# Kernel tuning notes

Hardware: AMD Instinct MI355X
Metric: run time of the kernel (lower is better)

Reference implementation:

```python
import jax, jax.numpy as jnp
import numpy as np

N_NODES = 100000
N_EDGES = 1600000
F_IN = 128
HID = 128
N_GRAPHS = 1024


def setup_inputs() -> dict:
    key = jax.random.key(0)
    ks = jax.random.split(key, 20)
    x = jax.random.normal(ks[0], (N_NODES, F_IN), dtype=jnp.float32)
    edge_index = jax.random.randint(ks[1], (2, N_EDGES), 0, N_NODES, dtype=jnp.int64)
    batch = jnp.sort(jax.random.randint(ks[2], (N_NODES,), 0, N_GRAPHS, dtype=jnp.int64))
    def lin(k, fi, fo):
        s = 1.0 / np.sqrt(fi)
        return jax.random.uniform(k, (fi, fo), jnp.float32, -s, s)
    params = {
        'W1': lin(ks[3], F_IN, HID), 'b1': jnp.zeros((HID,), jnp.float32),
        'W2': lin(ks[4], HID, HID), 'b2': jnp.zeros((HID,), jnp.float32),
        'W3': lin(ks[5], HID, HID), 'b3': jnp.zeros((HID,), jnp.float32),
        'W4': lin(ks[6], HID, HID), 'b4': jnp.zeros((HID,), jnp.float32),
        'W5': lin(ks[7], HID, HID), 'b5': jnp.zeros((HID,), jnp.float32),
        'beta1': jnp.ones((1,), jnp.float32),
        'beta2': jnp.ones((1,), jnp.float32),
        'Wl': lin(ks[8], HID, 1), 'bl': jnp.zeros((1,), jnp.float32),
    }
    return {'x': x, 'edge_index': edge_index, 'batch': batch, **params}


def _forward(x, src, dst, batch, W1, b1, W2, b2, W3, b3, W4, b4, W5, b5, beta1, beta2, Wl, bl):
    N = x.shape[0]
    # symmetric GCN normalization over A + I (shared by all GCNConv layers)
    deg = jax.ops.segment_sum(jnp.ones_like(dst, dtype=x.dtype), dst, num_segments=N)
    d_is = jnp.where(deg > 0, jax.lax.rsqrt(deg), 0.0)
    norm = d_is[src] * d_is[dst]  # [E+N]

    def gcn(h, W, b):
        m = (h @ W)[src] * norm[:, None]          # per-edge messages
        return jax.ops.segment_sum(m, dst, num_segments=N) + b

    def agnn(h, beta):
        nrm = jnp.maximum(jnp.linalg.norm(h, axis=1, keepdims=True), 1e-12)
        hn = h / nrm
        alpha = beta[0] * jnp.sum(hn[src] * hn[dst], axis=1)  # cosine sim per edge
        amax = jax.ops.segment_max(alpha, dst, num_segments=N)
        e = jnp.exp(alpha - amax[dst])
        denom = jax.ops.segment_sum(e, dst, num_segments=N)
        w = e / denom[dst]
        return jax.ops.segment_sum(h[src] * w[:, None], dst, num_segments=N)

    h = jnp.tanh(gcn(x, W1, b1))
    h = jnp.tanh(gcn(h, W2, b2))
    h = jnp.tanh(gcn(h, W3, b3))
    h = jnp.tanh(gcn(h, W4, b4))
    h = jnp.tanh(gcn(h, W5, b5))
    h = jnp.tanh(agnn(h, beta1))
    h = jnp.tanh(agnn(h, beta2))

    # global mean pool per graph
    sums = jax.ops.segment_sum(h, batch, num_segments=N_GRAPHS)
    cnts = jax.ops.segment_sum(jnp.ones((N,), h.dtype), batch, num_segments=N_GRAPHS)
    pooled = sums / jnp.maximum(cnts, 1.0)[:, None]

    # layer_norm over feature dim, no affine
    mu = jnp.mean(pooled, axis=-1, keepdims=True)
    var = jnp.mean(jnp.square(pooled - mu), axis=-1, keepdims=True)
    ln = (pooled - mu) * jax.lax.rsqrt(var + 1e-5)
    # dropout is identity in eval mode
    return ln @ Wl + bl


def reference(x, edge_index, batch, W1, b1, W2, b2, W3, b3, W4, b4, W5, b5, beta1, beta2, Wl, bl):
    N = x.shape[0]
    loops = jnp.arange(N, dtype=edge_index.dtype)
    src = jnp.concatenate([edge_index[0], loops])  # add self-loops (GCNConv & AGNNConv default)
    dst = jnp.concatenate([edge_index[1], loops])
    return _forward(x, src, dst, batch, W1, b1, W2, b2, W3, b3, W4, b4, W5, b5, beta1, beta2, Wl, bl)
```

## Files before the change

kernel.cpp:

```cpp
#include <hip/hip_runtime.h>
#include <hip/hip_fp16.h>
#include <math.h>

typedef _Float16 f16x8 __attribute__((ext_vector_type(8)));
typedef float f32x4 __attribute__((ext_vector_type(4)));

union U4H8 { uint4 u; f16x8 h; };

__device__ __forceinline__ void unpack8(uint4 u, float* f) {
    union { uint4 u; __half2 h2[4]; } U; U.u = u;
    float2 a = __half22float2(U.h2[0]);
    float2 b = __half22float2(U.h2[1]);
    float2 c = __half22float2(U.h2[2]);
    float2 d = __half22float2(U.h2[3]);
    f[0] = a.x; f[1] = a.y; f[2] = b.x; f[3] = b.y;
    f[4] = c.x; f[5] = c.y; f[6] = d.x; f[7] = d.y;
}

__global__ void k_zero_deg(int* deg, int N) {
    int i = blockIdx.x * blockDim.x + threadIdx.x;
    if (i < N) deg[i] = 0;
}

__global__ void k_count(const int* __restrict__ dst, int* deg, int* rank, int E) {
    int i = blockIdx.x * blockDim.x + threadIdx.x;
    if (i < E) rank[i] = atomicAdd(&deg[dst[i]], 1);
}

__global__ void k_dis(const int* __restrict__ deg, float* dis, int N) {
    int i = blockIdx.x * blockDim.x + threadIdx.x;
    if (i < N) dis[i] = rsqrtf((float)(deg[i] + 1));
}

__global__ void k_scan1(const int* __restrict__ deg, int* part, int N) {
    int base = blockIdx.x * 1024;
    int tid = threadIdx.x;
    int s = 0;
#pragma unroll
    for (int j = 0; j < 4; ++j) {
        int idx = base + tid * 4 + j;
        if (idx < N) s += deg[idx] + 1;
    }
    __shared__ int sm[256];
    sm[tid] = s;
    __syncthreads();
    for (int off = 128; off > 0; off >>= 1) {
        if (tid < off) sm[tid] += sm[tid + off];
        __syncthreads();
    }
    if (tid == 0) part[blockIdx.x] = sm[0];
}

__global__ void k_scan2(int* part, int nb, int* offs, int N) {
    if (blockIdx.x == 0 && threadIdx.x == 0) {
        int run = 0;
        for (int b = 0; b < nb; ++b) { int t = part[b]; part[b] = run; run += t; }
        offs[N] = run;
    }
}

__global__ void k_scan3(const int* __restrict__ deg, const int* __restrict__ part,
                        int* offs, int N) {
    __shared__ int sm[256];
    int base = blockIdx.x * 1024;
    int tid = threadIdx.x;
    int a[4];
    int s = 0;
#pragma unroll
    for (int j = 0; j < 4; ++j) {
        int idx = base + tid * 4 + j;
        a[j] = (idx < N) ? (deg[idx] + 1) : 0;
        s += a[j];
    }
    sm[tid] = s;
    __syncthreads();
    for (int off = 1; off < 256; off <<= 1) {
        int v = (tid >= off) ? sm[tid - off] : 0;
        __syncthreads();
        sm[tid] += v;
        __syncthreads();
    }
    int excl = sm[tid] - s + part[blockIdx.x];
#pragma unroll
    for (int j = 0; j < 4; ++j) {
        int idx = base + tid * 4 + j;
        if (idx < N) offs[idx] = excl;
        excl += a[j];
    }
}

__global__ void k_fill_edges(const int* __restrict__ ei, int E,
                             const int* __restrict__ offs,
                             const int* __restrict__ rank, int* csr) {
    int i = blockIdx.x * blockDim.x + threadIdx.x;
    if (i >= E) return;
    int s = ei[i], d = ei[E + i];
    csr[offs[d] + rank[i]] = s;
}

__global__ void k_fill_loops(const int* __restrict__ offs, int* csr, int N) {
    int n = blockIdx.x * blockDim.x + threadIdx.x;
    if (n < N) csr[offs[n + 1] - 1] = n;
}

__global__ void k_gstart(const int* __restrict__ batch, int N, int* gstart, int G) {
    int g = blockIdx.x * blockDim.x + threadIdx.x;
    if (g > G) return;
    int lo = 0, hi = N;
    while (lo < hi) {
        int mid = (lo + hi) >> 1;
        if (batch[mid] < g) lo = mid + 1; else hi = mid;
    }
    gstart[g] = lo;
}

__global__ __launch_bounds__(256) void k_cast(
    const float* __restrict__ x, const float* __restrict__ dis,
    __half* __restrict__ hx, int npairs)
{
    int i = blockIdx.x * blockDim.x + threadIdx.x;
    if (i >= npairs) return;
    float2 v = ((const float2*)x)[i];
    float d = dis[i >> 6];
    ((__half2*)hx)[i] = __floats2half2_rn(d * v.x, d * v.y);
}

__global__ void k_prepw(const float* __restrict__ W, __half* __restrict__ wt_hi,
                        __half* __restrict__ wt_lo) {
    int t = blockIdx.x * 256 + threadIdx.x;
    int j = t & 7, q = t >> 3;
    int l15 = q & 15, nt = (q >> 4) & 7;
    int lg = (q >> 7) & 3, ks = q >> 9;
    int n = nt * 16 + l15, k = ks * 32 + lg * 8 + j;
    float w = W[k * 128 + n];
    __half hi = __float2half_rn(w);
    wt_hi[t] = hi;
    wt_lo[t] = __float2half_rn(w - __half2float(hi));
}

__global__ __launch_bounds__(256) void k_gcn_agg(
    const __half* __restrict__ g, const int* __restrict__ csr,
    const int* __restrict__ offs, const float* __restrict__ dis,
    __half* __restrict__ agg, int N)
{
    int node = (blockIdx.x * blockDim.x + threadIdx.x) >> 4;
    int l = threadIdx.x & 15;
    if (node >= N) return;
    int j0 = offs[node], j1 = offs[node + 1];
    float dd = dis[node];
    const uint4* hp = (const uint4*)g + l;
    float acc[8] = {0.f, 0.f, 0.f, 0.f, 0.f, 0.f, 0.f, 0.f};
    int j = j0;
    for (; j + 4 <= j1; j += 4) {
        int s0 = csr[j + 0], s1 = csr[j + 1], s2 = csr[j + 2], s3 = csr[j + 3];
        uint4 u0 = hp[(size_t)s0 * 16];
        uint4 u1 = hp[(size_t)s1 * 16];
        uint4 u2 = hp[(size_t)s2 * 16];
        uint4 u3 = hp[(size_t)s3 * 16];
        float f0[8], f1[8], f2[8], f3[8];
        unpack8(u0, f0); unpack8(u1, f1); unpack8(u2, f2); unpack8(u3, f3);
#pragma unroll
        for (int i = 0; i < 8; ++i)
            acc[i] += f0[i] + f1[i] + f2[i] + f3[i];
    }
    for (; j < j1; ++j) {
        int s = csr[j];
        uint4 u = hp[(size_t)s * 16];
        float f[8]; unpack8(u, f);
#pragma unroll
        for (int i = 0; i < 8; ++i) acc[i] += f[i];
    }
    union { uint4 u; __half2 h2[4]; } P;
    P.h2[0] = __floats2half2_rn(dd * acc[0], dd * acc[1]);
    P.h2[1] = __floats2half2_rn(dd * acc[2], dd * acc[3]);
    P.h2[2] = __floats2half2_rn(dd * acc[4], dd * acc[5]);
    P.h2[3] = __floats2half2_rn(dd * acc[6], dd * acc[7]);
    ((uint4*)agg)[(size_t)node * 16 + l] = P.u;
}

#define GEMM_STG_OFF 65536
#define GEMM_STG_STRIDE 72
#define GEMM_LDS_BYTES (65536 + 8 * 16 * GEMM_STG_STRIDE)

__global__ __launch_bounds__(512) void k_gemm_mfma(
    const __half* __restrict__ in, const __half* __restrict__ wt_hi,
    const __half* __restrict__ wt_lo, const float* __restrict__ bias,
    const float* __restrict__ scale, __half* __restrict__ out,
    int ntiles, int nrows, float* __restrict__ invn_out)
{
    extern __shared__ char smem[];
    uint4* wlds = (uint4*)smem;
    int tid = threadIdx.x;
    int wv = tid >> 6;
    char* stg = smem + GEMM_STG_OFF + wv * 16 * GEMM_STG_STRIDE;

    {
        const uint4* sh = (const uint4*)wt_hi;
        const uint4* sl = (const uint4*)wt_lo;
        for (int t = tid; t < 2048; t += 512) {
            wlds[t] = sh[t];
            wlds[t + 2048] = sl[t];
        }
    }
    __syncthreads();

    int lane = tid & 63;
    int l15 = lane & 15, lg = lane >> 4;

    f32x4 bv[8];
#pragma unroll
    for (int nt = 0; nt < 8; ++nt)
        bv[nt] = *(const f32x4*)(bias + nt * 16 + lg * 4);

    int wid = blockIdx.x * 8 + wv;
    int t0 = wid * 2;
    for (int tile = t0; tile < t0 + 2 && tile < ntiles; ++tile) {
        int row0 = tile * 16;
        int row = row0 + l15;
        if (row >= nrows) row = nrows - 1;

        U4H8 b[4];
        const uint4* ap = (const uint4*)(in + (size_t)row * 128);
#pragma unroll
        for (int ks = 0; ks < 4; ++ks) b[ks].u = ap[ks * 4 + lg];

        f32x4 acc[8];
#pragma unroll
        for (int nt = 0; nt < 8; ++nt) acc[nt] = (f32x4){0.f, 0.f, 0.f, 0.f};

#pragma unroll
        for (int ks = 0; ks < 4; ++ks) {
#pragma unroll
            for (int nt = 0; nt < 8; ++nt) {
                int fi = (ks * 4 + lg) * 128 + nt * 16 + l15;
                U4H8 ah; ah.u = wlds[fi];
                U4H8 al; al.u = wlds[fi + 2048];
                acc[nt] = __builtin_amdgcn_mfma_f32_16x16x32_f16(ah.h, b[ks].h, acc[nt], 0, 0, 0);
                acc[nt] = __builtin_amdgcn_mfma_f32_16x16x32_f16(al.h, b[ks].h, acc[nt], 0, 0, 0);
            }
        }

        float sc = scale ? scale[row] : 1.0f;
        float sq = 0.f;
        int node = lane >> 2, sub = lane & 3;
#pragma unroll
        for (int np = 0; np < 4; ++np) {
#pragma unroll
            for (int h = 0; h < 2; ++h) {
                int nt = np * 2 + h;
                float o[4];
#pragma unroll
                for (int r = 0; r < 4; ++r) {
                    float xv = acc[nt][r] + bv[nt][r];
                    float e = __expf(xv + xv);
                    o[r] = 1.f - 2.f / (e + 1.f);
                    sq += o[r] * o[r];
                }
                union { __half2 h2[2]; uint2 u; } pk;
                pk.h2[0] = __floats2half2_rn(sc * o[0], sc * o[1]);
                pk.h2[1] = __floats2half2_rn(sc * o[2], sc * o[3]);
                *(uint2*)(stg + l15 * GEMM_STG_STRIDE + h * 32 + lg * 8) = pk.u;
            }
            uint4 v = *(const uint4*)(stg + node * GEMM_STG_STRIDE + sub * 16);
            if (row0 + node < nrows)
                *(uint4*)(out + (size_t)(row0 + node) * 128 + np * 32 + sub * 8) = v;
        }
        if (invn_out) {
            sq += __shfl_xor(sq, 16, 64);
            sq += __shfl_xor(sq, 32, 64);
            if (lg == 0) invn_out[row] = 1.0f / fmaxf(sqrtf(sq), 1e-12f);
        }
    }
}

__global__ __launch_bounds__(256) void k_agnn(
    const __half* __restrict__ h, const int* __restrict__ csr,
    const int* __restrict__ offs, const float* __restrict__ invn,
    const float* __restrict__ beta_p, __half* __restrict__ out, int N,
    float* __restrict__ invn_out)
{
    int node = (blockIdx.x * blockDim.x + threadIdx.x) >> 4;
    int l = threadIdx.x & 15;
    if (node >= N) return;
    int j0 = offs[node], j1 = offs[node + 1];
    const uint4* hp = (const uint4*)h + l;
    float hd[8]; unpack8(hp[(size_t)node * 16], hd);
    float bi = beta_p[0] * invn[node];
    float denom = 0.f;
    float acc[8] = {0.f, 0.f, 0.f, 0.f, 0.f, 0.f, 0.f, 0.f};
    int j = j0;
    for (; j + 2 <= j1; j += 2) {
        int s0 = csr[j], s1 = csr[j + 1];
        float in0 = invn[s0], in1 = invn[s1];
        uint4 u0 = hp[(size_t)s0 * 16];
        uint4 u1 = hp[(size_t)s1 * 16];
        float f0[8], f1[8];
        unpack8(u0, f0); unpack8(u1, f1);
        float d0 = 0.f, d1 = 0.f;
#pragma unroll
        for (int i = 0; i < 8; ++i) { d0 += f0[i] * hd[i]; d1 += f1[i] * hd[i]; }
#pragma unroll
        for (int off = 1; off < 16; off <<= 1) {
            d0 += __shfl_xor(d0, off, 64);
            d1 += __shfl_xor(d1, off, 64);
        }
        float p0 = __expf(bi * in0 * d0);
        float p1 = __expf(bi * in1 * d1);
        denom += p0 + p1;
#pragma unroll
        for (int i = 0; i < 8; ++i) acc[i] += p0 * f0[i] + p1 * f1[i];
    }
    for (; j < j1; ++j) {
        int s = csr[j];
        float ins = invn[s];
        uint4 u = hp[(size_t)s * 16];
        float f[8]; unpack8(u, f);
        float d = 0.f;
#pragma unroll
        for (int i = 0; i < 8; ++i) d += f[i] * hd[i];
#pragma unroll
        for (int off = 1; off < 16; off <<= 1) d += __shfl_xor(d, off, 64);
        float p = __expf(bi * ins * d);
        denom += p;
#pragma unroll
        for (int i = 0; i < 8; ++i) acc[i] += p * f[i];
    }
    float inv = 1.0f / denom;
    float o[8];
#pragma unroll
    for (int i = 0; i < 8; ++i) o[i] = tanhf(acc[i] * inv);
    union { uint4 u; __half2 h2[4]; } P;
    P.h2[0] = __floats2half2_rn(o[0], o[1]);
    P.h2[1] = __floats2half2_rn(o[2], o[3]);
    P.h2[2] = __floats2half2_rn(o[4], o[5]);
    P.h2[3] = __floats2half2_rn(o[6], o[7]);
    ((uint4*)out)[(size_t)node * 16 + l] = P.u;
    if (invn_out) {
        float s2 = 0.f;
#pragma unroll
        for (int i = 0; i < 8; ++i) s2 += o[i] * o[i];
#pragma unroll
        for (int off = 1; off < 16; off <<= 1) s2 += __shfl_xor(s2, off, 64);
        if (l == 0) invn_out[node] = 1.0f / fmaxf(sqrtf(s2), 1e-12f);
    }
}

__global__ __launch_bounds__(256) void k_pool(
    const __half* __restrict__ h, const int* __restrict__ gstart,
    const float* __restrict__ Wl, const float* __restrict__ bl,
    float* __restrict__ out, int G)
{
    int g = (blockIdx.x * blockDim.x + threadIdx.x) >> 4;
    int l = threadIdx.x & 15;
    if (g >= G) return;
    int s = gstart[g], e = gstart[g + 1];
    const uint4* hp = (const uint4*)h + l;
    float acc[8] = {0.f, 0.f, 0.f, 0.f, 0.f, 0.f, 0.f, 0.f};
    for (int n = s; n < e; ++n) {
        float f[8]; unpack8(hp[(size_t)n * 16], f);
#pragma unroll
        for (int i = 0; i < 8; ++i) acc[i] += f[i];
    }
    float inv = 1.0f / fmaxf((float)(e - s), 1.0f);
#pragma unroll
    for (int i = 0; i < 8; ++i) acc[i] *= inv;
    float part = 0.f;
#pragma unroll
    for (int i = 0; i < 8; ++i) part += acc[i];
#pragma unroll
    for (int off = 1; off < 16; off <<= 1) part += __shfl_xor(part, off, 64);
    float mu = part * (1.0f / 128.0f);
    float vpart = 0.f;
#pragma unroll
    for (int i = 0; i < 8; ++i) { float d = acc[i] - mu; vpart += d * d; }
#pragma unroll
    for (int off = 1; off < 16; off <<= 1) vpart += __shfl_xor(vpart, off, 64);
    float r = rsqrtf(vpart * (1.0f / 128.0f) + 1e-5f);
    float4 w0 = *(const float4*)(Wl + l * 8);
    float4 w1 = *(const float4*)(Wl + l * 8 + 4);
    float wv[8] = {w0.x, w0.y, w0.z, w0.w, w1.x, w1.y, w1.z, w1.w};
    float dot = 0.f;
#pragma unroll
    for (int i = 0; i < 8; ++i) dot += (acc[i] - mu) * r * wv[i];
#pragma unroll
    for (int off = 1; off < 16; off <<= 1) dot += __shfl_xor(dot, off, 64);
    if (l == 0) out[g] = dot + bl[0];
}

extern "C" void kernel_launch(void* const* d_in, const int* in_sizes, int n_in,
                              void* d_out, int out_size, void* d_ws, size_t ws_size,
                              hipStream_t stream) {
    const float* x  = (const float*)d_in[0];
    const int* ei   = (const int*)d_in[1];
    const int* batch = (const int*)d_in[2];
    const float* Ws[5] = {(const float*)d_in[3], (const float*)d_in[5],
                          (const float*)d_in[7], (const float*)d_in[9],
                          (const float*)d_in[11]};
    const float* bs[5] = {(const float*)d_in[4], (const float*)d_in[6],
                          (const float*)d_in[8], (const float*)d_in[10],
                          (const float*)d_in[12]};
    const float* beta1 = (const float*)d_in[13];
    const float* beta2 = (const float*)d_in[14];
    const float* Wl = (const float*)d_in[15];
    const float* bl = (const float*)d_in[16];
    float* out = (float*)d_out;

    int N = in_sizes[0] / 128;
    int E = in_sizes[1] / 2;
    int G = out_size;

    char* ws = (char*)d_ws;
    size_t off = 0;
    auto alloc = [&](size_t bytes) -> void* {
        void* p = ws + off;
        off = (off + bytes + 255) & ~(size_t)255;
        return p;
    };
    __half* aggh = (__half*)alloc((size_t)N * 128 * 2);
    __half* hA   = (__half*)alloc((size_t)N * 128 * 2);
    __half* hB   = (__half*)alloc((size_t)N * 128 * 2);
    int*   deg   = (int*)alloc((size_t)N * 4);
    int*   offs  = (int*)alloc((size_t)(N + 1) * 4);
    int*   rank  = (int*)alloc((size_t)E * 4);
    int*   csr   = (int*)alloc((size_t)(E + N) * 4);
    float* dis   = (float*)alloc((size_t)N * 4);
    float* invn  = (float*)alloc((size_t)N * 4);
    float* invn2 = (float*)alloc((size_t)N * 4);
    __half* wtHi = (__half*)alloc((size_t)5 * 16384 * 2);
    __half* wtLo = (__half*)alloc((size_t)5 * 16384 * 2);
    int nb = (N + 1023) / 1024;
    int*   part  = (int*)alloc((size_t)nb * 4);
    int*   gst   = (int*)alloc((size_t)(G + 1) * 4);

    k_zero_deg<<<(N + 255) / 256, 256, 0, stream>>>(deg, N);
    k_count<<<(E + 255) / 256, 256, 0, stream>>>(ei + E, deg, rank, E);
    k_dis<<<(N + 255) / 256, 256, 0, stream>>>(deg, dis, N);
    k_scan1<<<nb, 256, 0, stream>>>(deg, part, N);
    k_scan2<<<1, 64, 0, stream>>>(part, nb, offs, N);
    k_scan3<<<nb, 256, 0, stream>>>(deg, part, offs, N);
    k_fill_edges<<<(E + 255) / 256, 256, 0, stream>>>(ei, E, offs, rank, csr);
    k_fill_loops<<<(N + 255) / 256, 256, 0, stream>>>(offs, csr, N);
    k_gstart<<<(G + 1 + 255) / 256, 256, 0, stream>>>(batch, N, gst, G);
    k_cast<<<(N * 64 + 255) / 256, 256, 0, stream>>>(x, dis, hA, N * 64);
    for (int l = 0; l < 5; ++l)
        k_prepw<<<64, 256, 0, stream>>>(Ws[l], wtHi + l * 16384, wtLo + l * 16384);

    int aggBlocks = (N + 15) / 16;
    int ntiles = (N + 15) / 16;
    int gemmBlocks = (ntiles + 15) / 16;

    const __half* hin = hA;
    __half* hout = hB;
    for (int l = 0; l < 5; ++l) {
        k_gcn_agg<<<aggBlocks, 256, 0, stream>>>(hin, csr, offs, dis, aggh, N);
        k_gemm_mfma<<<gemmBlocks, 512, GEMM_LDS_BYTES, stream>>>(
            aggh, wtHi + l * 16384, wtLo + l * 16384, bs[l],
            (l < 4) ? dis : nullptr, hout, ntiles, N,
            (l == 4) ? invn : nullptr);
        const __half* t = hin; hin = hout; hout = (__half*)t;
    }
    k_agnn<<<aggBlocks, 256, 0, stream>>>(hin, csr, offs, invn, beta1, hout, N, invn2);
    k_agnn<<<aggBlocks, 256, 0, stream>>>(hout, csr, offs, invn2, beta2, (__half*)hin, N, nullptr);
    k_pool<<<(G + 15) / 16, 256, 0, stream>>>(hin, gst, Wl, bl, out, G);
}
```

Baseline: 744.8 us.

## Assign a full wavefront per node in GCN and AGNN gather kernels

Both neighbor-aggregation kernels now map one 64-lane wavefront per node instead of 16 lanes. The four 16-lane slots each process two neighbors per iteration and then combine partial sums via cross-lane shuffles. The aim is more outstanding gathers per node and lower per-node latency in these memory-bound kernels. In exchange, lanes are masked on tail iterations and there are four times as many waves. The AGNN padding adds tiny exp(-100) terms to the softmax denominator.

```diff
diff --git a/kernel.cpp b/kernel.cpp
--- a/kernel.cpp
+++ b/kernel.cpp
@@ -6,6 +6,7 @@
 typedef float f32x4 __attribute__((ext_vector_type(4)));
 
 union U4H8 { uint4 u; f16x8 h; };
+union U4H { uint4 u; __half h[8]; __half2 h2[4]; };
 
 __device__ __forceinline__ void unpack8(uint4 u, float* f) {
     union { uint4 u; __half2 h2[4]; } U; U.u = u;
@@ -143,39 +144,42 @@
     const int* __restrict__ offs, const float* __restrict__ dis,
     __half* __restrict__ agg, int N)
 {
-    int node = (blockIdx.x * blockDim.x + threadIdx.x) >> 4;
-    int l = threadIdx.x & 15;
+    int node = (blockIdx.x * blockDim.x + threadIdx.x) >> 6;
+    int lane = threadIdx.x & 63;
+    int l15 = lane & 15, slot = lane >> 4;
     if (node >= N) return;
     int j0 = offs[node], j1 = offs[node + 1];
     float dd = dis[node];
-    const uint4* hp = (const uint4*)g + l;
+    const uint4* h4 = (const uint4*)g;
     float acc[8] = {0.f, 0.f, 0.f, 0.f, 0.f, 0.f, 0.f, 0.f};
-    int j = j0;
-    for (; j + 4 <= j1; j += 4) {
-        int s0 = csr[j + 0], s1 = csr[j + 1], s2 = csr[j + 2], s3 = csr[j + 3];
-        uint4 u0 = hp[(size_t)s0 * 16];
-        uint4 u1 = hp[(size_t)s1 * 16];
-        uint4 u2 = hp[(size_t)s2 * 16];
-        uint4 u3 = hp[(size_t)s3 * 16];
-        float f0[8], f1[8], f2[8], f3[8];
-        unpack8(u0, f0); unpack8(u1, f1); unpack8(u2, f2); unpack8(u3, f3);
-#pragma unroll
-        for (int i = 0; i < 8; ++i)
-            acc[i] += f0[i] + f1[i] + f2[i] + f3[i];
-    }
-    for (; j < j1; ++j) {
-        int s = csr[j];
-        uint4 u = hp[(size_t)s * 16];
-        float f[8]; unpack8(u, f);
-#pragma unroll
-        for (int i = 0; i < 8; ++i) acc[i] += f[i];
-    }
-    union { uint4 u; __half2 h2[4]; } P;
-    P.h2[0] = __floats2half2_rn(dd * acc[0], dd * acc[1]);
-    P.h2[1] = __floats2half2_rn(dd * acc[2], dd * acc[3]);
-    P.h2[2] = __floats2half2_rn(dd * acc[4], dd * acc[5]);
-    P.h2[3] = __floats2half2_rn(dd * acc[6], dd * acc[7]);
-    ((uint4*)agg)[(size_t)node * 16 + l] = P.u;
+    for (int jb = j0; jb < j1; jb += 8) {
+        int i0 = jb + slot * 2, i1 = i0 + 1;
+        bool v0 = i0 < j1, v1 = i1 < j1;
+        int c0 = v0 ? i0 : j0, c1 = v1 ? i1 : j0;
+        int s0 = csr[c0], s1 = csr[c1];
+        uint4 u0 = h4[(unsigned)(s0 * 16 + l15)];
+        uint4 u1 = h4[(unsigned)(s1 * 16 + l15)];
+        float m0 = v0 ? 1.f : 0.f, m1 = v1 ? 1.f : 0.f;
+        U4H A, B; A.u = u0; B.u = u1;
+#pragma unroll
+        for (int i = 0; i < 8; ++i) {
+            acc[i] = fmaf(__half2float(A.h[i]), m0, acc[i]);
+            acc[i] = fmaf(__half2float(B.h[i]), m1, acc[i]);
+        }
+    }
+#pragma unroll
+    for (int i = 0; i < 8; ++i) {
+        acc[i] += __shfl_xor(acc[i], 16, 64);
+        acc[i] += __shfl_xor(acc[i], 32, 64);
+    }
+    if (slot == 0) {
+        union { uint4 u; __half2 h2[4]; } P;
+        P.h2[0] = __floats2half2_rn(dd * acc[0], dd * acc[1]);
+        P.h2[1] = __floats2half2_rn(dd * acc[2], dd * acc[3]);
+        P.h2[2] = __floats2half2_rn(dd * acc[4], dd * acc[5]);
+        P.h2[3] = __floats2half2_rn(dd * acc[6], dd * acc[7]);
+        ((uint4*)agg)[(unsigned)(node * 16 + l15)] = P.u;
+    }
 }
 
 #define GEMM_STG_OFF 65536
@@ -279,69 +283,76 @@
     const float* __restrict__ beta_p, __half* __restrict__ out, int N,
     float* __restrict__ invn_out)
 {
-    int node = (blockIdx.x * blockDim.x + threadIdx.x) >> 4;
-    int l = threadIdx.x & 15;
+    int node = (blockIdx.x * blockDim.x + threadIdx.x) >> 6;
+    int lane = threadIdx.x & 63;
+    int l15 = lane & 15, slot = lane >> 4;
     if (node >= N) return;
     int j0 = offs[node], j1 = offs[node + 1];
-    const uint4* hp = (const uint4*)h + l;
-    float hd[8]; unpack8(hp[(size_t)node * 16], hd);
+    const uint4* h4 = (const uint4*)h;
+    U4H D; D.u = h4[(unsigned)(node * 16 + l15)];
+    float hd[8];
+#pragma unroll
+    for (int i = 0; i < 8; ++i) hd[i] = __half2float(D.h[i]);
     float bi = beta_p[0] * invn[node];
     float denom = 0.f;
     float acc[8] = {0.f, 0.f, 0.f, 0.f, 0.f, 0.f, 0.f, 0.f};
-    int j = j0;
-    for (; j + 2 <= j1; j += 2) {
-        int s0 = csr[j], s1 = csr[j + 1];
+    for (int jb = j0; jb < j1; jb += 8) {
+        int i0 = jb + slot * 2, i1 = i0 + 1;
+        bool v0 = i0 < j1, v1 = i1 < j1;
+        int c0 = v0 ? i0 : j0, c1 = v1 ? i1 : j0;
+        int s0 = csr[c0], s1 = csr[c1];
         float in0 = invn[s0], in1 = invn[s1];
-        uint4 u0 = hp[(size_t)s0 * 16];
-        uint4 u1 = hp[(size_t)s1 * 16];
-        float f0[8], f1[8];
-        unpack8(u0, f0); unpack8(u1, f1);
+        uint4 u0 = h4[(unsigned)(s0 * 16 + l15)];
+        uint4 u1 = h4[(unsigned)(s1 * 16 + l15)];
+        U4H A, B; A.u = u0; B.u = u1;
         float d0 = 0.f, d1 = 0.f;
 #pragma unroll
-        for (int i = 0; i < 8; ++i) { d0 += f0[i] * hd[i]; d1 += f1[i] * hd[i]; }
+        for (int i = 0; i < 8; ++i) {
+            d0 = fmaf(__half2float(A.h[i]), hd[i], d0);
+            d1 = fmaf(__half2float(B.h[i]), hd[i], d1);
+        }
 #pragma unroll
         for (int off = 1; off < 16; off <<= 1) {
             d0 += __shfl_xor(d0, off, 64);
             d1 += __shfl_xor(d1, off, 64);
         }
-        float p0 = __expf(bi * in0 * d0);
-        float p1 = __expf(bi * in1 * d1);
+        float a0 = v0 ? bi * in0 * d0 : -100.f;
+        float a1 = v1 ? bi * in1 * d1 : -100.f;
+        float p0 = __expf(a0);
+        float p1 = __expf(a1);
         denom += p0 + p1;
 #pragma unroll
-        for (int i = 0; i < 8; ++i) acc[i] += p0 * f0[i] + p1 * f1[i];
-    }
-    for (; j < j1; ++j) {
-        int s = csr[j];
-        float ins = invn[s];
-        uint4 u = hp[(size_t)s * 16];
-        float f[8]; unpack8(u, f);
-        float d = 0.f;
-#pragma unroll
-        for (int i = 0; i < 8; ++i) d += f[i] * hd[i];
-#pragma unroll
-        for (int off = 1; off < 16; off <<= 1) d += __shfl_xor(d, off, 64);
-        float p = __expf(bi * ins * d);
-        denom += p;
-#pragma unroll
-        for (int i = 0; i < 8; ++i) acc[i] += p * f[i];
+        for (int i = 0; i < 8; ++i) {
+            acc[i] = fmaf(__half2float(A.h[i]), p0, acc[i]);
+            acc[i] = fmaf(__half2float(B.h[i]), p1, acc[i]);
+        }
+    }
+    denom += __shfl_xor(denom, 16, 64);
+    denom += __shfl_xor(denom, 32, 64);
+#pragma unroll
+    for (int i = 0; i < 8; ++i) {
+        acc[i] += __shfl_xor(acc[i], 16, 64);
+        acc[i] += __shfl_xor(acc[i], 32, 64);
     }
     float inv = 1.0f / denom;
     float o[8];
 #pragma unroll
     for (int i = 0; i < 8; ++i) o[i] = tanhf(acc[i] * inv);
-    union { uint4 u; __half2 h2[4]; } P;
-    P.h2[0] = __floats2half2_rn(o[0], o[1]);
-    P.h2[1] = __floats2half2_rn(o[2], o[3]);
-    P.h2[2] = __floats2half2_rn(o[4], o[5]);
-    P.h2[3] = __floats2half2_rn(o[6], o[7]);
-    ((uint4*)out)[(size_t)node * 16 + l] = P.u;
-    if (invn_out) {
-        float s2 = 0.f;
-#pragma unroll
-        for (int i = 0; i < 8; ++i) s2 += o[i] * o[i];
-#pragma unroll
-        for (int off = 1; off < 16; off <<= 1) s2 += __shfl_xor(s2, off, 64);
-        if (l == 0) invn_out[node] = 1.0f / fmaxf(sqrtf(s2), 1e-12f);
+    if (slot == 0) {
+        union { uint4 u; __half2 h2[4]; } P;
+        P.h2[0] = __floats2half2_rn(o[0], o[1]);
+        P.h2[1] = __floats2half2_rn(o[2], o[3]);
+        P.h2[2] = __floats2half2_rn(o[4], o[5]);
+        P.h2[3] = __floats2half2_rn(o[6], o[7]);
+        ((uint4*)out)[(unsigned)(node * 16 + l15)] = P.u;
+        if (invn_out) {
+            float s2 = 0.f;
+#pragma unroll
+            for (int i = 0; i < 8; ++i) s2 += o[i] * o[i];
+#pragma unroll
+            for (int off = 1; off < 16; off <<= 1) s2 += __shfl_xor(s2, off, 64);
+            if (l15 == 0) invn_out[node] = 1.0f / fmaxf(sqrtf(s2), 1e-12f);
+        }
     }
 }
 
@@ -445,7 +456,7 @@
     for (int l = 0; l < 5; ++l)
         k_prepw<<<64, 256, 0, stream>>>(Ws[l], wtHi + l * 16384, wtLo + l * 16384);
 
-    int aggBlocks = (N + 15) / 16;
+    int aggBlocks = (N + 3) / 4;
     int ntiles = (N + 15) / 16;
     int gemmBlocks = (ntiles + 15) / 16;
 
```

Measured after the change: 742.5 us. Within noise of the previous version (-0.3%).
